# Performance work log

Hardware: AMD Instinct MI355X
Metric: run time of the kernel (lower is better)

Reference implementation:

```python
import jax, jax.numpy as jnp
import numpy as np

N_USERS = 100000
N_ITEMS = 50000
N_NODES = N_USERS + N_ITEMS
NNZ = 4800000
DIM = 64
N_HOPS = 3
EPS = 0.1
PERTURBED = True


def setup_inputs() -> dict:
    key = jax.random.key(0)
    k1, k2, k3, k4, k5 = jax.random.split(key, 5)
    user_embed = jax.random.normal(k1, (N_USERS, DIM), dtype=jnp.float32) * 0.1
    item_embed = jax.random.normal(k2, (N_ITEMS, DIM), dtype=jnp.float32) * 0.1
    adj_rows = jax.random.randint(k3, (NNZ,), 0, N_NODES, dtype=jnp.int32)
    adj_cols = jax.random.randint(k4, (NNZ,), 0, N_NODES, dtype=jnp.int32)
    # scale values ~ 1/avg_degree so repeated propagation stays well-conditioned
    adj_vals = jax.random.uniform(k5, (NNZ,), dtype=jnp.float32) * (1.0 / 32.0)
    return {"user_embed": user_embed, "item_embed": item_embed,
            "adj_rows": adj_rows, "adj_cols": adj_cols, "adj_vals": adj_vals}


def _spmm(rows, cols, vals, x):
    # sparse [N,N] @ dense [N,D] via gather + segment-sum
    msgs = vals[:, None] * x[cols]  # [nnz, D]
    return jax.ops.segment_sum(msgs, rows, num_segments=N_NODES)


def _forward(user_embed, item_embed, adj_rows, adj_cols, adj_vals):
    ego = jnp.concatenate([user_embed, item_embed], axis=0)  # [N, D]
    noise_key = jax.random.key(42)
    all_embeddings = []
    layer_embeddings = ego
    for k in range(N_HOPS):
        ego = _spmm(adj_rows, adj_cols, adj_vals, ego)
        if PERTURBED:
            noise = jax.random.uniform(jax.random.fold_in(noise_key, k), ego.shape, dtype=ego.dtype)
            noise = noise / jnp.linalg.norm(noise, axis=-1, keepdims=True)  # F.normalize dim=-1
            ego = ego + jnp.sign(ego) * noise * EPS
        all_embeddings.append(ego)
        if k == 0:
            layer_embeddings = ego
    all_mean = jnp.mean(jnp.stack(all_embeddings, axis=1), axis=1)  # [N, D]
    user_all, item_all = all_mean[:N_USERS], all_mean[N_USERS:]
    user_layer, item_layer = layer_embeddings[:N_USERS], layer_embeddings[N_USERS:]
    return (user_all, item_all, user_layer, item_layer)


def reference(user_embed, item_embed, adj_rows, adj_cols, adj_vals):
    return _forward(user_embed, item_embed, adj_rows, adj_cols, adj_vals)
```

## Files before the change

### kernel.cpp

```cpp
#include <hip/hip_runtime.h>
#include <stdint.h>

#define N_USERS 100000
#define N_ITEMS 50000
#define N_NODES 150000
#define NNZ     4800000
#define DIM     64
#define NELEM   (N_NODES * DIM)
#define EPS_F   0.1f


#define NBUCK  768
#define RPB    196
#define BCAP   6752
#define CHUNK  8192
#define NCHUNK 586

#define E_MASK   0x7FFFFFu
#define COL_MASK 0x3FFFFu

typedef unsigned long long ull;

__host__ __device__ inline void threefry2x32_fn(unsigned k0, unsigned k1,
                                                unsigned x0, unsigned x1,
                                                unsigned* o0, unsigned* o1) {
  unsigned ks0 = k0, ks1 = k1, ks2 = k0 ^ k1 ^ 0x1BD11BDAu;
  x0 += ks0; x1 += ks1;
#define TF_ROUND(r) { x0 += x1; x1 = (x1 << (r)) | (x1 >> (32 - (r))); x1 ^= x0; }
  TF_ROUND(13) TF_ROUND(15) TF_ROUND(26) TF_ROUND(6)
  x0 += ks1; x1 += ks2 + 1u;
  TF_ROUND(17) TF_ROUND(29) TF_ROUND(16) TF_ROUND(24)
  x0 += ks2; x1 += ks0 + 2u;
  TF_ROUND(13) TF_ROUND(15) TF_ROUND(26) TF_ROUND(6)
  x0 += ks0; x1 += ks1 + 3u;
  TF_ROUND(17) TF_ROUND(29) TF_ROUND(16) TF_ROUND(24)
  x0 += ks1; x1 += ks2 + 4u;
  TF_ROUND(13) TF_ROUND(15) TF_ROUND(26) TF_ROUND(6)
  x0 += ks2; x1 += ks0 + 5u;
#undef TF_ROUND
  *o0 = x0; *o1 = x1;
}

__global__ void hist_kernel(const int* __restrict__ rows,
                            int* __restrict__ counts) {
  __shared__ int h[NBUCK];
  int c = blockIdx.x, tid = threadIdx.x;
  for (int t = tid; t < NBUCK; t += 256) h[t] = 0;
  __syncthreads();
  int cb = c * CHUNK;
  #pragma unroll
  for (int k = 0; k < CHUNK / 256; ++k) {
    int i = cb + k * 256 + tid;
    if (i < NNZ) {
      int r = rows[i];
      atomicAdd(&h[r / RPB], 1);
    }
  }
  __syncthreads();
  for (int t = tid; t < NBUCK; t += 256)
    counts[c * NBUCK + t] = h[t];
}

__global__ void scan_kernel(const int* __restrict__ counts,
                            int* __restrict__ base,
                            int* __restrict__ btot) {
  int b = blockIdx.x * 256 + threadIdx.x;
  int run = 0;
  #pragma unroll 8
  for (int c = 0; c < NCHUNK; ++c) {
    int v = counts[c * NBUCK + b];
    base[c * NBUCK + b] = run;
    run += v;
  }
  btot[b] = run;
}

__global__ void scatter_kernel(const int* __restrict__ rows,
                               const int* __restrict__ cols,
                               const int* __restrict__ base,
                               ull* __restrict__ staging) {
  __shared__ int cur[NBUCK];
  int c = blockIdx.x, tid = threadIdx.x;
  for (int t = tid; t < NBUCK; t += 256) cur[t] = base[c * NBUCK + t];
  __syncthreads();
  int cb = c * CHUNK;
  #pragma unroll
  for (int k = 0; k < CHUNK / 256; ++k) {
    int i = cb + k * 256 + tid;
    if (i < NNZ) {
      int r  = rows[i];
      int cc = cols[i];
      int b  = r / RPB;
      int lr = r - b * RPB;
      int p  = atomicAdd(&cur[b], 1);
      if (p < BCAP)
        staging[(long long)b * BCAP + p] =
            ((ull)(unsigned)lr << 41) | ((ull)(unsigned)cc << 23) | (unsigned)i;
    }
  }
}

__global__ void group_sort_kernel(const float* __restrict__ vals,
                                  const int* __restrict__ btot,
                                  ull* __restrict__ staging,
                                  int* __restrict__ cnt,
                                  int* __restrict__ off) {
  __shared__ ull B[BCAP];
  __shared__ int rowcnt[RPB];
  __shared__ int rowoff[RPB + 1];
  __shared__ int rowcur[RPB];
  int b = blockIdx.x, tid = threadIdx.x;
  int tot = btot[b]; if (tot > BCAP) tot = BCAP;
  ull* sg = staging + (long long)b * BCAP;

  for (int t = tid; t < RPB; t += 256) { rowcnt[t] = 0; rowcur[t] = 0; }
  __syncthreads();

  for (int s = tid; s < tot; s += 256) {
    ull v = sg[s];
    atomicAdd(&rowcnt[(int)(v >> 41)], 1);
  }
  __syncthreads();

  if (tid == 0) {
    int run = 0;
    for (int t = 0; t < RPB; ++t) { rowoff[t] = run; run += rowcnt[t]; }
    rowoff[RPB] = run;
  }
  __syncthreads();

  int row0 = b * RPB;
  for (int t = tid; t < RPB; t += 256) {
    int r = row0 + t;
    if (r < N_NODES) { cnt[r] = rowcnt[t]; off[r] = b * BCAP + rowoff[t]; }
  }

  for (int s = tid; s < tot; s += 256) {
    ull v = sg[s];
    int lr = (int)(v >> 41);
    int p = atomicAdd(&rowcur[lr], 1);
    B[rowoff[lr] + p] = v;
  }
  __syncthreads();

  for (int s = tid; s < tot; s += 256) {
    ull v = B[s];
    int lr = (int)(v >> 41);
    unsigned e = (unsigned)(v & E_MASK);
    int lo = rowoff[lr], hi = rowoff[lr + 1];
    int rk = 0;
    for (int j = lo; j < hi; ++j)
      rk += ((unsigned)(B[j] & E_MASK) < e) ? 1 : 0;
    float val = vals[e];
    unsigned col = (unsigned)((v >> 23) & COL_MASK);
    sg[lo + rk] = ((ull)col << 32) | __float_as_uint(val);
  }
}

template <int K>
__global__ void spmm_noise_kernel(const ull* __restrict__ pairs,
                                  const int* __restrict__ cnt,
                                  const int* __restrict__ off,
                                  const float* __restrict__ user_e,
                                  const float* __restrict__ item_e,
                                  const float* __restrict__ src,
                                  float* __restrict__ dst,
                                  float* __restrict__ out_mean,
                                  unsigned key0, unsigned key1) {
  int wid  = threadIdx.x >> 6;
  int lane = threadIdx.x & 63;
  int row  = blockIdx.x * 4 + wid;
  int row_u = __builtin_amdgcn_readfirstlane(row);
  int d = cnt[row_u];
  if (d > 128) d = 128;
  const ull* prow = pairs + off[row_u];

  #define GATHER(c, xout_) do {                                            \
    if (K == 0) {                                                          \
      const float* bp_ = ((c) < N_USERS)                                   \
          ? user_e + (long long)(c) * DIM                                  \
          : item_e + (long long)((c) - N_USERS) * DIM;                     \
      xout_ = bp_[lane];                                                   \
    } else {                                                               \
      xout_ = src[(long long)(c) * DIM + lane];                            \
    }                                                                      \
  } while (0)

  float acc = 0.0f;
  for (int t = 0; t < d; t += 8) {
    int i0 = t,     i1 = t + 1, i2 = t + 2, i3 = t + 3;
    int i4 = t + 4, i5 = t + 5, i6 = t + 6, i7 = t + 7;
    int dm1 = d - 1;
    if (i1 > dm1) i1 = dm1;  if (i2 > dm1) i2 = dm1;  if (i3 > dm1) i3 = dm1;
    if (i4 > dm1) i4 = dm1;  if (i5 > dm1) i5 = dm1;  if (i6 > dm1) i6 = dm1;
    if (i7 > dm1) i7 = dm1;
    ull p0 = prow[i0], p1 = prow[i1], p2 = prow[i2], p3 = prow[i3];
    ull p4 = prow[i4], p5 = prow[i5], p6 = prow[i6], p7 = prow[i7];
    int c0 = (int)(unsigned)(p0 >> 32), c1 = (int)(unsigned)(p1 >> 32);
    int c2 = (int)(unsigned)(p2 >> 32), c3 = (int)(unsigned)(p3 >> 32);
    int c4 = (int)(unsigned)(p4 >> 32), c5 = (int)(unsigned)(p5 >> 32);
    int c6 = (int)(unsigned)(p6 >> 32), c7 = (int)(unsigned)(p7 >> 32);
    float x0, x1, x2, x3, x4, x5, x6, x7;
    GATHER(c0, x0); GATHER(c1, x1); GATHER(c2, x2); GATHER(c3, x3);
    GATHER(c4, x4); GATHER(c5, x5); GATHER(c6, x6); GATHER(c7, x7);
    float v0 = __uint_as_float((unsigned)(p0 & 0xffffffffu));
    float v1 = (t + 1 < d) ? __uint_as_float((unsigned)(p1 & 0xffffffffu)) : 0.0f;
    float v2 = (t + 2 < d) ? __uint_as_float((unsigned)(p2 & 0xffffffffu)) : 0.0f;
    float v3 = (t + 3 < d) ? __uint_as_float((unsigned)(p3 & 0xffffffffu)) : 0.0f;
    float v4 = (t + 4 < d) ? __uint_as_float((unsigned)(p4 & 0xffffffffu)) : 0.0f;
    float v5 = (t + 5 < d) ? __uint_as_float((unsigned)(p5 & 0xffffffffu)) : 0.0f;
    float v6 = (t + 6 < d) ? __uint_as_float((unsigned)(p6 & 0xffffffffu)) : 0.0f;
    float v7 = (t + 7 < d) ? __uint_as_float((unsigned)(p7 & 0xffffffffu)) : 0.0f;
    acc = __fadd_rn(acc, __fmul_rn(v0, x0));
    acc = __fadd_rn(acc, __fmul_rn(v1, x1));
    acc = __fadd_rn(acc, __fmul_rn(v2, x2));
    acc = __fadd_rn(acc, __fmul_rn(v3, x3));
    acc = __fadd_rn(acc, __fmul_rn(v4, x4));
    acc = __fadd_rn(acc, __fmul_rn(v5, x5));
    acc = __fadd_rn(acc, __fmul_rn(v6, x6));
    acc = __fadd_rn(acc, __fmul_rn(v7, x7));
  }
  #undef GATHER

  int i = row * DIM + lane;
  unsigned o0, o1;
  threefry2x32_fn(key0, key1, 0u, (unsigned)i, &o0, &o1);
  unsigned bits = o0 ^ o1;
  float u = __uint_as_float((bits >> 9) | 0x3f800000u) - 1.0f;
  float ss = __fmul_rn(u, u);
  #pragma unroll
  for (int offs = 32; offs >= 1; offs >>= 1)
    ss += __shfl_xor(ss, offs, 64);
  float noise = u / sqrtf(ss);
  float s = (acc > 0.0f) ? 1.0f : ((acc < 0.0f) ? -1.0f : 0.0f);
  float val = __fadd_rn(acc, __fmul_rn(s, __fmul_rn(noise, EPS_F)));

  if (K == 0) {
    dst[i] = val;
    out_mean[i] = val;
  } else if (K == 1) {
    dst[i] = val;
    out_mean[i] = __fadd_rn(out_mean[i], val);
  } else {
    out_mean[i] = __fadd_rn(out_mean[i], val) / 3.0f;
  }
}

extern "C" void kernel_launch(void* const* d_in, const int* in_sizes, int n_in,
                              void* d_out, int out_size, void* d_ws, size_t ws_size,
                              hipStream_t stream) {
  const float* user_e = (const float*)d_in[0];
  const float* item_e = (const float*)d_in[1];
  const int*   rows   = (const int*)d_in[2];
  const int*   cols   = (const int*)d_in[3];
  const float* vals   = (const float*)d_in[4];

  float* out_mean  = (float*)d_out;
  float* out_layer = (float*)d_out + NELEM;

  char* w = (char*)d_ws;
  ull*   staging = (ull*)w;
  int*   counts  = (int*)(w + 41484288);
  int*   basep   = (int*)(w + 43284480);
  int*   btot    = (int*)(w + 45084672);
  int*   cnt     = (int*)(w + 45087744);
  int*   off     = (int*)(w + 45687744);
  float* ego     = (float*)(w + 46287744);

  unsigned hk0[3], hk1[3];
  for (int k = 0; k < 3; ++k)
    threefry2x32_fn(0u, 42u, 0u, (unsigned)k, &hk0[k], &hk1[k]);

  const int BT = 256;
  const unsigned row_blocks = N_NODES / 4;

  hist_kernel<<<NCHUNK, BT, 0, stream>>>(rows, counts);
  scan_kernel<<<NBUCK / BT, BT, 0, stream>>>(counts, basep, btot);
  scatter_kernel<<<NCHUNK, BT, 0, stream>>>(rows, cols, basep, staging);
  group_sort_kernel<<<NBUCK, BT, 0, stream>>>(vals, btot, staging, cnt, off);

  spmm_noise_kernel<0><<<row_blocks, BT, 0, stream>>>(
      staging, cnt, off, user_e, item_e, nullptr, out_layer, out_mean, hk0[0], hk1[0]);
  spmm_noise_kernel<1><<<row_blocks, BT, 0, stream>>>(
      staging, cnt, off, nullptr, nullptr, out_layer, ego, out_mean, hk0[1], hk1[1]);
  spmm_noise_kernel<2><<<row_blocks, BT, 0, stream>>>(
      staging, cnt, off, nullptr, nullptr, ego, nullptr, out_mean, hk0[2], hk1[2]);
}
```

Measured before the change: 946.9 us.

## Scatter edges into chunk-local bucket segments and gather them per bucket into LDS

The scatter pass now writes each chunk's edges into a contiguous chunk-local region, ordered by bucket, using a new per-chunk prefix scan. Before, each edge went straight into a global per-bucket staging area. group_sort then pulls each bucket's pieces from every chunk into shared memory and writes the sorted pairs to a separate buffer. The aim is more local, coalesced scatter writes. Chunk size is doubled, and the SpMM inner loop now issues 16 gathers per iteration instead of 8, to expose more memory-level parallelism. The cost is an extra kernel, a second LDS buffer of roughly 54KB that may reduce group_sort occupancy, and small scattered segment reads during the per-bucket gather.

```diff
diff --git a/kernel.cpp b/kernel.cpp
--- a/kernel.cpp
+++ b/kernel.cpp
@@ -13,8 +13,8 @@
 #define NBUCK  768
 #define RPB    196
 #define BCAP   6752
-#define CHUNK  8192
-#define NCHUNK 586
+#define CHUNK  16384
+#define NCHUNK 293
 
 #define E_MASK   0x7FFFFFu
 #define COL_MASK 0x3FFFFu
@@ -48,7 +48,7 @@
   for (int t = tid; t < NBUCK; t += 256) h[t] = 0;
   __syncthreads();
   int cb = c * CHUNK;
-  #pragma unroll
+  #pragma unroll 4
   for (int k = 0; k < CHUNK / 256; ++k) {
     int i = cb + k * 256 + tid;
     if (i < NNZ) {
@@ -61,9 +61,9 @@
     counts[c * NBUCK + t] = h[t];
 }
 
-__global__ void scan_kernel(const int* __restrict__ counts,
-                            int* __restrict__ base,
-                            int* __restrict__ btot) {
+__global__ void scanB_kernel(const int* __restrict__ counts,
+                             int* __restrict__ base,
+                             int* __restrict__ btot) {
   int b = blockIdx.x * 256 + threadIdx.x;
   int run = 0;
   #pragma unroll 8
@@ -75,16 +75,45 @@
   btot[b] = run;
 }
 
+__global__ void scanC_kernel(const int* __restrict__ counts,
+                             int* __restrict__ off2) {
+  int wid = threadIdx.x >> 6, lane = threadIdx.x & 63;
+  int c = blockIdx.x * 4 + wid;
+  if (c >= NCHUNK) return;
+  const int* cc = counts + c * NBUCK;
+  int* oo = off2 + c * NBUCK;
+  int loc[12];
+  int sum = 0;
+  #pragma unroll
+  for (int j = 0; j < 12; ++j) {
+    int v = cc[lane * 12 + j];
+    loc[j] = sum; sum += v;
+  }
+  int pref = 0;
+  for (int k = 0; k < 64; ++k) {
+    int sk = __shfl(sum, k, 64);
+    if (k < lane) pref += sk;
+  }
+  int base0 = c * CHUNK + pref;
+  #pragma unroll
+  for (int j = 0; j < 12; ++j)
+    oo[lane * 12 + j] = base0 + loc[j];
+}
+
 __global__ void scatter_kernel(const int* __restrict__ rows,
                                const int* __restrict__ cols,
-                               const int* __restrict__ base,
-                               ull* __restrict__ staging) {
+                               const int* __restrict__ off2,
+                               ull* __restrict__ staging2) {
+  __shared__ int obase[NBUCK];
   __shared__ int cur[NBUCK];
   int c = blockIdx.x, tid = threadIdx.x;
-  for (int t = tid; t < NBUCK; t += 256) cur[t] = base[c * NBUCK + t];
+  for (int t = tid; t < NBUCK; t += 256) {
+    obase[t] = off2[c * NBUCK + t];
+    cur[t] = 0;
+  }
   __syncthreads();
   int cb = c * CHUNK;
-  #pragma unroll
+  #pragma unroll 4
   for (int k = 0; k < CHUNK / 256; ++k) {
     int i = cb + k * 256 + tid;
     if (i < NNZ) {
@@ -93,33 +122,45 @@
       int b  = r / RPB;
       int lr = r - b * RPB;
       int p  = atomicAdd(&cur[b], 1);
-      if (p < BCAP)
-        staging[(long long)b * BCAP + p] =
-            ((ull)(unsigned)lr << 41) | ((ull)(unsigned)cc << 23) | (unsigned)i;
+      staging2[obase[b] + p] =
+          ((ull)(unsigned)lr << 41) | ((ull)(unsigned)cc << 23) | (unsigned)i;
     }
   }
 }
 
 __global__ void group_sort_kernel(const float* __restrict__ vals,
+                                  const int* __restrict__ counts,
+                                  const int* __restrict__ base,
+                                  const int* __restrict__ off2,
                                   const int* __restrict__ btot,
-                                  ull* __restrict__ staging,
+                                  const ull* __restrict__ staging2,
+                                  ull* __restrict__ pairsF,
                                   int* __restrict__ cnt,
                                   int* __restrict__ off) {
   __shared__ ull B[BCAP];
+  __shared__ ull B2[BCAP];
   __shared__ int rowcnt[RPB];
   __shared__ int rowoff[RPB + 1];
   __shared__ int rowcur[RPB];
   int b = blockIdx.x, tid = threadIdx.x;
+  int wid = tid >> 6, lane = tid & 63;
+
+  for (int t = tid; t < RPB; t += 256) { rowcnt[t] = 0; rowcur[t] = 0; }
+
+  for (int c = wid; c < NCHUNK; c += 4) {
+    int len  = counts[c * NBUCK + b];
+    int src  = off2[c * NBUCK + b];
+    int dstB = base[c * NBUCK + b];
+    for (int j = lane; j < len; j += 64)
+      if (dstB + j < BCAP)
+        B[dstB + j] = staging2[src + j];
+  }
+  __syncthreads();
+
   int tot = btot[b]; if (tot > BCAP) tot = BCAP;
-  ull* sg = staging + (long long)b * BCAP;
-
-  for (int t = tid; t < RPB; t += 256) { rowcnt[t] = 0; rowcur[t] = 0; }
-  __syncthreads();
-
-  for (int s = tid; s < tot; s += 256) {
-    ull v = sg[s];
-    atomicAdd(&rowcnt[(int)(v >> 41)], 1);
-  }
+
+  for (int s = tid; s < tot; s += 256)
+    atomicAdd(&rowcnt[(int)(B[s] >> 41)], 1);
   __syncthreads();
 
   if (tid == 0) {
@@ -136,24 +177,24 @@
   }
 
   for (int s = tid; s < tot; s += 256) {
-    ull v = sg[s];
+    ull v = B[s];
     int lr = (int)(v >> 41);
     int p = atomicAdd(&rowcur[lr], 1);
-    B[rowoff[lr] + p] = v;
+    B2[rowoff[lr] + p] = v;
   }
   __syncthreads();
 
   for (int s = tid; s < tot; s += 256) {
-    ull v = B[s];
+    ull v = B2[s];
     int lr = (int)(v >> 41);
     unsigned e = (unsigned)(v & E_MASK);
     int lo = rowoff[lr], hi = rowoff[lr + 1];
     int rk = 0;
     for (int j = lo; j < hi; ++j)
-      rk += ((unsigned)(B[j] & E_MASK) < e) ? 1 : 0;
+      rk += ((unsigned)(B2[j] & E_MASK) < e) ? 1 : 0;
     float val = vals[e];
     unsigned col = (unsigned)((v >> 23) & COL_MASK);
-    sg[lo + rk] = ((ull)col << 32) | __float_as_uint(val);
+    pairsF[(long long)b * BCAP + lo + rk] = ((ull)col << 32) | __float_as_uint(val);
   }
 }
 
@@ -187,38 +228,25 @@
   } while (0)
 
   float acc = 0.0f;
-  for (int t = 0; t < d; t += 8) {
-    int i0 = t,     i1 = t + 1, i2 = t + 2, i3 = t + 3;
-    int i4 = t + 4, i5 = t + 5, i6 = t + 6, i7 = t + 7;
+  for (int t = 0; t < d; t += 16) {
     int dm1 = d - 1;
-    if (i1 > dm1) i1 = dm1;  if (i2 > dm1) i2 = dm1;  if (i3 > dm1) i3 = dm1;
-    if (i4 > dm1) i4 = dm1;  if (i5 > dm1) i5 = dm1;  if (i6 > dm1) i6 = dm1;
-    if (i7 > dm1) i7 = dm1;
-    ull p0 = prow[i0], p1 = prow[i1], p2 = prow[i2], p3 = prow[i3];
-    ull p4 = prow[i4], p5 = prow[i5], p6 = prow[i6], p7 = prow[i7];
-    int c0 = (int)(unsigned)(p0 >> 32), c1 = (int)(unsigned)(p1 >> 32);
-    int c2 = (int)(unsigned)(p2 >> 32), c3 = (int)(unsigned)(p3 >> 32);
-    int c4 = (int)(unsigned)(p4 >> 32), c5 = (int)(unsigned)(p5 >> 32);
-    int c6 = (int)(unsigned)(p6 >> 32), c7 = (int)(unsigned)(p7 >> 32);
-    float x0, x1, x2, x3, x4, x5, x6, x7;
-    GATHER(c0, x0); GATHER(c1, x1); GATHER(c2, x2); GATHER(c3, x3);
-    GATHER(c4, x4); GATHER(c5, x5); GATHER(c6, x6); GATHER(c7, x7);
-    float v0 = __uint_as_float((unsigned)(p0 & 0xffffffffu));
-    float v1 = (t + 1 < d) ? __uint_as_float((unsigned)(p1 & 0xffffffffu)) : 0.0f;
-    float v2 = (t + 2 < d) ? __uint_as_float((unsigned)(p2 & 0xffffffffu)) : 0.0f;
-    float v3 = (t + 3 < d) ? __uint_as_float((unsigned)(p3 & 0xffffffffu)) : 0.0f;
-    float v4 = (t + 4 < d) ? __uint_as_float((unsigned)(p4 & 0xffffffffu)) : 0.0f;
-    float v5 = (t + 5 < d) ? __uint_as_float((unsigned)(p5 & 0xffffffffu)) : 0.0f;
-    float v6 = (t + 6 < d) ? __uint_as_float((unsigned)(p6 & 0xffffffffu)) : 0.0f;
-    float v7 = (t + 7 < d) ? __uint_as_float((unsigned)(p7 & 0xffffffffu)) : 0.0f;
-    acc = __fadd_rn(acc, __fmul_rn(v0, x0));
-    acc = __fadd_rn(acc, __fmul_rn(v1, x1));
-    acc = __fadd_rn(acc, __fmul_rn(v2, x2));
-    acc = __fadd_rn(acc, __fmul_rn(v3, x3));
-    acc = __fadd_rn(acc, __fmul_rn(v4, x4));
-    acc = __fadd_rn(acc, __fmul_rn(v5, x5));
-    acc = __fadd_rn(acc, __fmul_rn(v6, x6));
-    acc = __fadd_rn(acc, __fmul_rn(v7, x7));
+    ull p[16];
+    #pragma unroll
+    for (int j = 0; j < 16; ++j) {
+      int i = t + j; if (i > dm1) i = dm1;
+      p[j] = prow[i];
+    }
+    float x[16];
+    #pragma unroll
+    for (int j = 0; j < 16; ++j) {
+      int c = (int)(unsigned)(p[j] >> 32);
+      GATHER(c, x[j]);
+    }
+    #pragma unroll
+    for (int j = 0; j < 16; ++j) {
+      float v = (t + j < d) ? __uint_as_float((unsigned)(p[j] & 0xffffffffu)) : 0.0f;
+      acc = __fadd_rn(acc, __fmul_rn(v, x[j]));
+    }
   }
   #undef GATHER
 
@@ -259,13 +287,15 @@
   float* out_layer = (float*)d_out + NELEM;
 
   char* w = (char*)d_ws;
-  ull*   staging = (ull*)w;
-  int*   counts  = (int*)(w + 41484288);
-  int*   basep   = (int*)(w + 43284480);
-  int*   btot    = (int*)(w + 45084672);
-  int*   cnt     = (int*)(w + 45087744);
-  int*   off     = (int*)(w + 45687744);
-  float* ego     = (float*)(w + 46287744);
+  ull*   staging2 = (ull*)w;
+  ull*   pairsF   = (ull*)(w + 38404096);
+  int*   counts   = (int*)(w + 79888384);
+  int*   basep    = (int*)(w + 80788480);
+  int*   off2     = (int*)(w + 81688576);
+  int*   btot     = (int*)(w + 82588672);
+  int*   cnt      = (int*)(w + 82591744);
+  int*   off      = (int*)(w + 83191744);
+  float* ego      = (float*)w;
 
   unsigned hk0[3], hk1[3];
   for (int k = 0; k < 3; ++k)
@@ -275,14 +305,16 @@
   const unsigned row_blocks = N_NODES / 4;
 
   hist_kernel<<<NCHUNK, BT, 0, stream>>>(rows, counts);
-  scan_kernel<<<NBUCK / BT, BT, 0, stream>>>(counts, basep, btot);
-  scatter_kernel<<<NCHUNK, BT, 0, stream>>>(rows, cols, basep, staging);
-  group_sort_kernel<<<NBUCK, BT, 0, stream>>>(vals, btot, staging, cnt, off);
+  scanB_kernel<<<NBUCK / BT, BT, 0, stream>>>(counts, basep, btot);
+  scanC_kernel<<<(NCHUNK + 3) / 4, BT, 0, stream>>>(counts, off2);
+  scatter_kernel<<<NCHUNK, BT, 0, stream>>>(rows, cols, off2, staging2);
+  group_sort_kernel<<<NBUCK, BT, 0, stream>>>(vals, counts, basep, off2, btot,
+                                              staging2, pairsF, cnt, off);
 
   spmm_noise_kernel<0><<<row_blocks, BT, 0, stream>>>(
-      staging, cnt, off, user_e, item_e, nullptr, out_layer, out_mean, hk0[0], hk1[0]);
+      pairsF, cnt, off, user_e, item_e, nullptr, out_layer, out_mean, hk0[0], hk1[0]);
   spmm_noise_kernel<1><<<row_blocks, BT, 0, stream>>>(
-      staging, cnt, off, nullptr, nullptr, out_layer, ego, out_mean, hk0[1], hk1[1]);
+      pairsF, cnt, off, nullptr, nullptr, out_layer, ego, out_mean, hk0[1], hk1[1]);
   spmm_noise_kernel<2><<<row_blocks, BT, 0, stream>>>(
-      staging, cnt, off, nullptr, nullptr, ego, nullptr, out_mean, hk0[2], hk1[2]);
-}
+      pairsF, cnt, off, nullptr, nullptr, ego, nullptr, out_mean, hk0[2], hk1[2]);
+}
```

After: 1.192 ms. 1.26x slower.
